# Optimization experiments

Hardware: AMD Instinct MI355X
Metric: run time of the kernel (lower is better)

Reference implementation:

```python
import jax, jax.numpy as jnp
import numpy as np

TEMP = 0.07
BASE_TEMP = 0.07
NUM_HEADS = 8


def setup_inputs() -> dict:
    key = jax.random.key(0)
    k1, k2, k3 = jax.random.split(key, 3)
    B, B2, V, E, C = 1024, 2048, 2, 512, 64
    features = jax.random.normal(k1, (B, V, E), dtype=jnp.float32)
    additional_negatives = jax.random.normal(k2, (B2, V, E), dtype=jnp.float32)
    labels = jax.random.bernoulli(k3, 0.05, (B, C)).astype(jnp.float32)
    return {"features": features, "additional_negatives": additional_negatives, "labels": labels}


def _l2norm(x, eps=1e-12):
    # matches torch.nn.functional.normalize (norm clamped at eps)
    n = jnp.linalg.norm(x, axis=-1, keepdims=True)
    return x / jnp.maximum(n, eps)


def reference(features, additional_negatives, labels):
    B, V, E = features.shape
    H = NUM_HEADS
    F = E // H
    N = B * V

    mask0 = (labels @ labels.T) > 0  # (B, B) label-overlap mask

    # torch.cat(torch.unbind(x, dim=1), dim=0): view-major concat -> (N, E)
    f = jnp.transpose(features, (1, 0, 2)).reshape(N, E).reshape(N, H, F)
    neg = jnp.transpose(additional_negatives, (1, 0, 2))
    M = neg.shape[0] * neg.shape[1]
    neg = neg.reshape(M, E // 1).reshape(M, H, F)

    f = _l2norm(f)
    neg = _l2norm(neg)

    # per-head pairwise similarities (the diagonal(dim1=2,dim2=3) of the full
    # (N,H,N,H) product keeps only matching heads -> einsum over shared h)
    D = jnp.einsum('ihf,jhf->ijh', f, f)      # (N, N, H)
    DN = jnp.einsum('ihf,mhf->imh', f, neg)   # (N, M, H)

    heads = jnp.argmax(D, axis=-1)            # (N, N) per-pair best head

    D = D / TEMP
    DN = DN / TEMP

    # The original builds L[i,k,j] = D[i,j,heads[i,k]]; its max over j and the
    # masked exp-sums depend only on (i, heads[i,k]), so compute per (i, h).
    m1 = jax.lax.stop_gradient(jnp.max(D, axis=1))   # (N, H) = max_j D[i,j,h]
    m2 = jax.lax.stop_gradient(jnp.max(DN, axis=1))  # (N, H) = max_m DN[i,m,h]

    not_self = 1.0 - jnp.eye(N, dtype=D.dtype)       # exclude j == i
    S1 = jnp.sum(jnp.exp(D - m1[:, None, :]) * not_self[:, :, None], axis=1)  # (N, H)
    S2 = jnp.sum(jnp.exp(DN - m2[:, None, :]), axis=1)                         # (N, H)

    # note: original sums exp terms referenced to DIFFERENT maxes (m1 vs m2);
    # reproduce that exactly.
    denom = m1 + jnp.log(S1 + S2)                    # (N, H)

    # diagonal term: D[i,k,heads[i,k]] == max_h D[i,k,h]
    Dmax = jnp.max(D, axis=-1)                       # (N, N)
    denom_ik = jnp.take_along_axis(denom, heads, axis=1)  # (N, N)
    log_prob = Dmax - denom_ik                       # (N, N)

    mask = jnp.tile(mask0, (V, V)).astype(D.dtype) * not_self  # (N, N)
    mean_log_prob_pos = jnp.sum(mask * log_prob, axis=1) / jnp.sum(mask, axis=1)
    loss_vec = -(TEMP / BASE_TEMP) * mean_log_prob_pos          # (N,)

    finite = jnp.isfinite(loss_vec)
    cnt = jnp.sum(finite.astype(loss_vec.dtype))
    loss = jnp.sum(jnp.where(finite, loss_vec, 0.0)) / cnt
    loss = jnp.where(jnp.isnan(loss), jnp.zeros((), loss.dtype), loss)
    return loss
```

## Files before the change

kernel.cpp:

```cpp
#include <hip/hip_runtime.h>

typedef unsigned long long u64;
typedef unsigned short ushort_t;
typedef __bf16 bf16x8 __attribute__((ext_vector_type(8)));
typedef float f32x4 __attribute__((ext_vector_type(4)));

#define NROWS 2048
#define MROWS 4096
#define BLAB  1024
#define INVT  (1.0f / 0.07f)
#define K2    (INVT * 1.4426950408889634f)

__device__ __forceinline__ bf16x8 ldb(const ushort_t* p) {
  return __builtin_bit_cast(bf16x8, *(const uint4*)p);
}

__device__ __forceinline__ ushort_t f2bf(float f) {
  unsigned u = __float_as_uint(f);
  u += 0x7fff + ((u >> 16) & 1);
  return (ushort_t)(u >> 16);
}

__global__ void k_prep(const float* __restrict__ feat, const float* __restrict__ negs,
                       const float* __restrict__ labels,
                       ushort_t* __restrict__ fnb, ushort_t* __restrict__ nnb,
                       u64* __restrict__ lbits, float* __restrict__ zbuf) {
  if (blockIdx.x >= 3072) {
    const int gtid = (blockIdx.x - 3072) * 256 + threadIdx.x;
    if (gtid < 4096) zbuf[gtid] = 0.0f;
    const int wid  = gtid >> 6;
    const int lane = threadIdx.x & 63;
    if (wid < BLAB) {
      float v = labels[wid * 64 + lane];
      u64 msk = __ballot(v != 0.0f);
      if (lane == 0) lbits[wid] = msk;
    }
    return;
  }
  const int wid  = blockIdx.x * 4 + ((threadIdx.x >> 6));
  const int lane = threadIdx.x & 63;
  const int g = lane >> 4, ln = lane & 15;
  const int p = wid * 4 + g;
  const float* src;
  ushort_t* dst;
  if (p < NROWS * 8) {
    const int i = p >> 3, h = p & 7;
    const int b = i & (BLAB - 1), v = i >> 10;
    src = feat + (b * 2 + v) * 512 + h * 64;
    dst = fnb + (h * NROWS + i) * 64;
  } else {
    const int q = p - NROWS * 8;
    const int m = q >> 3, h = q & 7;
    const int b2 = m & 2047, v = m >> 11;
    src = negs + (b2 * 2 + v) * 512 + h * 64;
    dst = nnb + (h * MROWS + m) * 64;
  }
  const float4 x = *(const float4*)(src + 4 * ln);
  float ss = x.x * x.x + x.y * x.y + x.z * x.z + x.w * x.w;
#pragma unroll
  for (int d = 1; d < 16; d <<= 1) ss += __shfl_xor(ss, d, 64);
  const float inv = 1.0f / fmaxf(sqrtf(ss), 1e-12f);
  ushort4 o;
  o.x = f2bf(x.x * inv); o.y = f2bf(x.y * inv);
  o.z = f2bf(x.z * inv); o.w = f2bf(x.w * inv);
  *(ushort4*)(dst + 4 * ln) = o;
}

__device__ __forceinline__ void store_ms4(float mc[4][4], float sa[4][4],
                                          float* __restrict__ gm, float* __restrict__ gs,
                                          int base, int off, int lg, int ln) {
#pragma unroll
  for (int rs = 0; rs < 4; ++rs) {
#pragma unroll
    for (int q = 0; q < 4; ++q) {
      float m = mc[rs][q], s = sa[rs][q];
#pragma unroll
      for (int d = 1; d < 16; d <<= 1) {
        m = fmaxf(m, __shfl_xor(m, d, 64));
        s += __shfl_xor(s, d, 64);
      }
      if (ln == 0) {
        const int row = base + rs * 16 + lg * 4 + q;
        gm[row * 128 + off] = m * INVT;
        gs[row * 128 + off] = s * exp2f((1.0f - m) * K2);
      }
      mc[rs][q] = -3.0e38f; sa[rs][q] = 0.0f;
    }
  }
}

__global__ __launch_bounds__(256, 2) void k_passA(const ushort_t* __restrict__ fnb,
                                                  const ushort_t* __restrict__ nnb,
                                                  float* __restrict__ m1p, float* __restrict__ S1p,
                                                  float* __restrict__ m2p, float* __restrict__ S2p) {
  const int tid  = threadIdx.x;
  const int head = blockIdx.x & 7;
  const int rbk  = (blockIdx.x >> 3) & 7;
  const int js   = blockIdx.x >> 6;
  const int w = tid >> 6, lane = tid & 63, lg = lane >> 4, ln = lane & 15;
  const ushort_t* fh = fnb + head * (NROWS * 64);
  const ushort_t* nh = nnb + head * (MROWS * 64);
  const int base = rbk * 256 + w * 64;
  const int off  = head * 16 + js;
  const int j0 = js * 128;
  const int t0 = js * 256;

  bf16x8 a0[4], a1[4];
#pragma unroll
  for (int rs = 0; rs < 4; ++rs) {
    const ushort_t* ap = fh + (base + rs * 16 + ln) * 64 + lg * 8;
    a0[rs] = ldb(ap); a1[rs] = ldb(ap + 32);
  }
  float mc[4][4], sa[4][4];
#pragma unroll
  for (int rs = 0; rs < 4; ++rs)
#pragma unroll
    for (int q = 0; q < 4; ++q) { mc[rs][q] = -3.0e38f; sa[rs][q] = 0.0f; }

#define TPTR(tt) ((tt) < 8 ? fh + (j0 + (tt) * 16 + ln) * 64 : nh + (t0 + ((tt) - 8) * 16 + ln) * 64)
#define NPTR(tt) (nh + (t0 + ((tt) - 8) * 16 + ln) * 64)
#define LOADT(PA, PB, tt) { const ushort_t* np_ = TPTR(tt); PA = *(const uint4*)(np_ + lg * 8); PB = *(const uint4*)(np_ + 32 + lg * 8); }
#define LOADN(PA, PB, tt) { const ushort_t* np_ = NPTR(tt); PA = *(const uint4*)(np_ + lg * 8); PB = *(const uint4*)(np_ + 32 + lg * 8); }

#define STEP(Pa, Pb, gjb, SELF)                                                              \
  {                                                                                          \
    _Pragma("unroll") for (int rs = 0; rs < 4; ++rs) {                                       \
      f32x4 c = {0.0f, 0.0f, 0.0f, 0.0f};                                                    \
      c = __builtin_amdgcn_mfma_f32_16x16x32_bf16(a0[rs], __builtin_bit_cast(bf16x8, Pa), c, 0, 0, 0); \
      c = __builtin_amdgcn_mfma_f32_16x16x32_bf16(a1[rs], __builtin_bit_cast(bf16x8, Pb), c, 0, 0, 0); \
      _Pragma("unroll") for (int q = 0; q < 4; ++q) {                                        \
        const float cv = c[q];                                                               \
        mc[rs][q] = fmaxf(mc[rs][q], cv);                                                    \
        float e = exp2f(fmaf(cv, K2, -K2));                                                  \
        if (SELF && (base + rs * 16 + lg * 4 + q == (gjb) + ln)) e = 0.0f;                   \
        sa[rs][q] += e;                                                                      \
      }                                                                                      \
    }                                                                                        \
  }

  uint4 P0a, P0b, P1a, P1b, P2a, P2b, P3a, P3b;
  LOADT(P0a, P0b, 0); LOADT(P1a, P1b, 1); LOADT(P2a, P2b, 2); LOADT(P3a, P3b, 3);

#pragma unroll 1
  for (int jj = 0; jj < 8; jj += 4) {
    STEP(P0a, P0b, j0 + jj * 16, 1);        LOADT(P0a, P0b, jj + 4);
    STEP(P1a, P1b, j0 + (jj + 1) * 16, 1);  LOADT(P1a, P1b, jj + 5);
    STEP(P2a, P2b, j0 + (jj + 2) * 16, 1);  LOADT(P2a, P2b, jj + 6);
    STEP(P3a, P3b, j0 + (jj + 3) * 16, 1);  LOADT(P3a, P3b, jj + 7);
  }
  store_ms4(mc, sa, m1p, S1p, base, off, lg, ln);

#pragma unroll 1
  for (int kk = 8; kk < 20; kk += 4) {
    STEP(P0a, P0b, 0, 0);  LOADN(P0a, P0b, kk + 4);
    STEP(P1a, P1b, 0, 0);  LOADN(P1a, P1b, kk + 5);
    STEP(P2a, P2b, 0, 0);  LOADN(P2a, P2b, kk + 6);
    STEP(P3a, P3b, 0, 0);  LOADN(P3a, P3b, kk + 7);
  }
  STEP(P0a, P0b, 0, 0);
  STEP(P1a, P1b, 0, 0);
  STEP(P2a, P2b, 0, 0);
  STEP(P3a, P3b, 0, 0);
  store_ms4(mc, sa, m2p, S2p, base, off, lg, ln);
#undef STEP
#undef LOADT
#undef LOADN
#undef TPTR
#undef NPTR
}

__global__ void k_denom(const float* __restrict__ m1p, const float* __restrict__ S1p,
                        const float* __restrict__ m2p, const float* __restrict__ S2p,
                        float* __restrict__ dnm) {
  const int e = blockIdx.x * 256 + threadIdx.x;
  const int row = e >> 3, h = e & 7;
  const int bidx = row * 128 + h * 16;
  float4 mq[4], sq[4], m2q[4], s2q[4];
#pragma unroll
  for (int k = 0; k < 4; ++k) {
    mq[k]  = *(const float4*)(m1p + bidx + 4 * k);
    sq[k]  = *(const float4*)(S1p + bidx + 4 * k);
    m2q[k] = *(const float4*)(m2p + bidx + 4 * k);
    s2q[k] = *(const float4*)(S2p + bidx + 4 * k);
  }
  float m = -3.0e38f, m2 = -3.0e38f;
#pragma unroll
  for (int k = 0; k < 4; ++k) {
    m  = fmaxf(m,  fmaxf(fmaxf(mq[k].x,  mq[k].y),  fmaxf(mq[k].z,  mq[k].w)));
    m2 = fmaxf(m2, fmaxf(fmaxf(m2q[k].x, m2q[k].y), fmaxf(m2q[k].z, m2q[k].w)));
  }
  float s = 0.0f, s2 = 0.0f;
#pragma unroll
  for (int k = 0; k < 4; ++k) {
    s  += sq[k].x  * __expf(mq[k].x  - m)  + sq[k].y  * __expf(mq[k].y  - m)
        + sq[k].z  * __expf(mq[k].z  - m)  + sq[k].w  * __expf(mq[k].w  - m);
    s2 += s2q[k].x * __expf(m2q[k].x - m2) + s2q[k].y * __expf(m2q[k].y - m2)
        + s2q[k].z * __expf(m2q[k].z - m2) + s2q[k].w * __expf(m2q[k].w - m2);
  }
  dnm[row * 8 + h] = m + __logf(s + s2);
}

__global__ __launch_bounds__(256, 2) void k_passB(const ushort_t* __restrict__ fnb,
                                                  const float* __restrict__ dnm,
                                                  const u64* __restrict__ lbits,
                                                  float* __restrict__ rowsum, float* __restrict__ rowcnt) {
  __shared__ float dn[64 * 9];
  const int tid = threadIdx.x;
  const int it = blockIdx.x >> 5, jt = blockIdx.x & 31;
  const int ibase = it * 64, jbase = jt * 64;
  const int w = tid >> 6, lane = tid & 63, lg = lane >> 4, ln = lane & 15;

  for (int e = tid; e < 512; e += 256) {
    const int il = e >> 3, h = e & 7;
    dn[il * 9 + h] = dnm[(ibase + il) * 8 + h];
  }
  __syncthreads();

  float dnr[4][8];
#pragma unroll
  for (int q = 0; q < 4; ++q) {
    const int il = w * 16 + lg * 4 + q;
#pragma unroll
    for (int h = 0; h < 8; ++h) dnr[q][h] = dn[il * 9 + h];
  }

  const int irow = ibase + w * 16 + ln;
  float maxd[4][4], bestdn[4][4];
#pragma unroll
  for (int sj = 0; sj < 4; ++sj)
#pragma unroll
    for (int q = 0; q < 4; ++q) { maxd[sj][q] = -3.0e38f; bestdn[sj][q] = 0.0f; }

#pragma unroll
  for (int h = 0; h < 8; ++h) {
    const ushort_t* fh = fnb + h * (NROWS * 64);
    const bf16x8 a0 = ldb(fh + irow * 64 + lg * 8);
    const bf16x8 a1 = ldb(fh + irow * 64 + 32 + lg * 8);
#pragma unroll
    for (int sj = 0; sj < 4; ++sj) {
      const int jrow = jbase + sj * 16 + ln;
      const bf16x8 b0 = ldb(fh + jrow * 64 + lg * 8);
      const bf16x8 b1 = ldb(fh + jrow * 64 + 32 + lg * 8);
      f32x4 c = {0.0f, 0.0f, 0.0f, 0.0f};
      c = __builtin_amdgcn_mfma_f32_16x16x32_bf16(a0, b0, c, 0, 0, 0);
      c = __builtin_amdgcn_mfma_f32_16x16x32_bf16(a1, b1, c, 0, 0, 0);
#pragma unroll
      for (int q = 0; q < 4; ++q)
        if (c[q] > maxd[sj][q]) { maxd[sj][q] = c[q]; bestdn[sj][q] = dnr[q][h]; }
    }
  }

  u64 lbi[4];
#pragma unroll
  for (int q = 0; q < 4; ++q) lbi[q] = lbits[(ibase + w * 16 + lg * 4 + q) & (BLAB - 1)];
  float rs[4] = {0, 0, 0, 0}, rc[4] = {0, 0, 0, 0};
#pragma unroll
  for (int sj = 0; sj < 4; ++sj) {
    const int gj = jbase + sj * 16 + ln;
    const u64 lbj = lbits[gj & (BLAB - 1)];
#pragma unroll
    for (int q = 0; q < 4; ++q) {
      const int gi = ibase + w * 16 + lg * 4 + q;
      if (gi != gj && (lbi[q] & lbj)) {
        rs[q] += maxd[sj][q] * INVT - bestdn[sj][q];
        rc[q] += 1.0f;
      }
    }
  }
#pragma unroll
  for (int q = 0; q < 4; ++q) {
#pragma unroll
    for (int d = 1; d < 16; d <<= 1) {
      rs[q] += __shfl_xor(rs[q], d, 64);
      rc[q] += __shfl_xor(rc[q], d, 64);
    }
  }
  if (ln == 0) {
#pragma unroll
    for (int q = 0; q < 4; ++q) {
      const int row = ibase + w * 16 + lg * 4 + q;
      atomicAdd(&rowsum[row], rs[q]);
      atomicAdd(&rowcnt[row], rc[q]);
    }
  }
}

__global__ void k_final(const float* __restrict__ rowsum, const float* __restrict__ rowcnt,
                        float* __restrict__ out) {
  __shared__ float sdata[4][2];
  const int tid = threadIdx.x;
  float s = 0.0f, c = 0.0f;
  for (int i = tid; i < NROWS; i += 256) {
    const float cnt = rowcnt[i];
    if (cnt > 0.0f) { s -= rowsum[i] / cnt; c += 1.0f; }
  }
#pragma unroll
  for (int d = 32; d; d >>= 1) { s += __shfl_xor(s, d, 64); c += __shfl_xor(c, d, 64); }
  const int w = tid >> 6;
  if ((tid & 63) == 0) { sdata[w][0] = s; sdata[w][1] = c; }
  __syncthreads();
  if (tid == 0) {
    s = 0.0f; c = 0.0f;
#pragma unroll
    for (int w2 = 0; w2 < 4; ++w2) { s += sdata[w2][0]; c += sdata[w2][1]; }
    out[0] = (c > 0.0f) ? s / c : 0.0f;
  }
}

extern "C" void kernel_launch(void* const* d_in, const int* in_sizes, int n_in,
                              void* d_out, int out_size, void* d_ws, size_t ws_size,
                              hipStream_t stream) {
  const float* feat   = (const float*)d_in[0];
  const float* negs   = (const float*)d_in[1];
  const float* labels = (const float*)d_in[2];
  float* out = (float*)d_out;

  ushort_t* fnb = (ushort_t*)d_ws;
  ushort_t* nnb = fnb + 8 * NROWS * 64;
  float* m1p = (float*)(nnb + 8 * MROWS * 64);
  float* S1p = m1p + NROWS * 128;
  float* m2p = S1p + NROWS * 128;
  float* S2p = m2p + NROWS * 128;
  float* rowsum = S2p + NROWS * 128;
  float* rowcnt = rowsum + 2048;
  u64*   lbits  = (u64*)(rowcnt + 2048);
  float* dnm    = (float*)(lbits + 1024);

  k_prep<<<3328, 256, 0, stream>>>(feat, negs, labels, fnb, nnb, lbits, rowsum);
  k_passA<<<1024, 256, 0, stream>>>(fnb, nnb, m1p, S1p, m2p, S2p);
  k_denom<<<64, 256, 0, stream>>>(m1p, S1p, m2p, S2p, dnm);
  k_passB<<<1024, 256, 0, stream>>>(fnb, dnm, lbits, rowsum, rowcnt);
  k_final<<<1, 256, 0, stream>>>(rowsum, rowcnt, out);
}
```

Measured before the change: 162.2 us.

## Stage passA B-tiles in swizzled LDS via direct global-to-LDS loads

Instead of each wave streaming the 24 key/negative tiles from global memory into registers with a 4-deep software prefetch, the block now loads all 24 tiles (48 KB) once into shared memory with global_load_lds and an XOR swizzle, then reads them from LDS inside the MFMA loop. This removes redundant per-wave global loads, since all 4 waves share the same B tiles, and avoids bank conflicts through the swizzle. In exchange it uses 48 KB of LDS per block, which may limit occupancy under the 2-blocks-per-SM launch bound. It also serializes all loads before compute with a full wait and barrier, so load latency is no longer overlapped with math.

```diff
diff --git a/kernel.cpp b/kernel.cpp
--- a/kernel.cpp
+++ b/kernel.cpp
@@ -93,6 +93,7 @@
                                                   const ushort_t* __restrict__ nnb,
                                                   float* __restrict__ m1p, float* __restrict__ S1p,
                                                   float* __restrict__ m2p, float* __restrict__ S2p) {
+  __shared__ ushort_t Bs[24 * 1024];
   const int tid  = threadIdx.x;
   const int head = blockIdx.x & 7;
   const int rbk  = (blockIdx.x >> 3) & 7;
@@ -105,6 +106,20 @@
   const int j0 = js * 128;
   const int t0 = js * 256;
 
+  {
+    const int pos  = tid & 127;
+    const int srow = pos >> 3;
+    const int sk   = pos & 7;
+    const int gsw  = (sk ^ (srow & 7)) * 8;
+    for (int r = 0; r < 12; ++r) {
+      const int tl = r * 2 + (tid >> 7);
+      const ushort_t* gsrc = (tl < 8 ? fh + (j0 + tl * 16 + srow) * 64
+                                     : nh + (t0 + (tl - 8) * 16 + srow) * 64) + gsw;
+      __builtin_amdgcn_global_load_lds((const unsigned int*)gsrc,
+                                       (unsigned int*)(Bs + tl * 1024 + pos * 8), 16, 0, 0);
+    }
+  }
+
   bf16x8 a0[4], a1[4];
 #pragma unroll
   for (int rs = 0; rs < 4; ++rs) {
@@ -117,13 +132,14 @@
 #pragma unroll
     for (int q = 0; q < 4; ++q) { mc[rs][q] = -3.0e38f; sa[rs][q] = 0.0f; }
 
-#define TPTR(tt) ((tt) < 8 ? fh + (j0 + (tt) * 16 + ln) * 64 : nh + (t0 + ((tt) - 8) * 16 + ln) * 64)
-#define NPTR(tt) (nh + (t0 + ((tt) - 8) * 16 + ln) * 64)
-#define LOADT(PA, PB, tt) { const ushort_t* np_ = TPTR(tt); PA = *(const uint4*)(np_ + lg * 8); PB = *(const uint4*)(np_ + 32 + lg * 8); }
-#define LOADN(PA, PB, tt) { const ushort_t* np_ = NPTR(tt); PA = *(const uint4*)(np_ + lg * 8); PB = *(const uint4*)(np_ + 32 + lg * 8); }
-
-#define STEP(Pa, Pb, gjb, SELF)                                                              \
+  asm volatile("s_waitcnt vmcnt(0)" ::: "memory");
+  __syncthreads();
+
+#define TCHUNK(tt, c) (Bs + (tt) * 1024 + (ln * 8 + ((c) ^ (ln & 7))) * 8)
+#define STEP(tt, gjb, SELF)                                                                  \
   {                                                                                          \
+    const uint4 Pa = *(const uint4*)TCHUNK(tt, lg);                                          \
+    const uint4 Pb = *(const uint4*)TCHUNK(tt, lg + 4);                                      \
     _Pragma("unroll") for (int rs = 0; rs < 4; ++rs) {                                       \
       f32x4 c = {0.0f, 0.0f, 0.0f, 0.0f};                                                    \
       c = __builtin_amdgcn_mfma_f32_16x16x32_bf16(a0[rs], __builtin_bit_cast(bf16x8, Pa), c, 0, 0, 0); \
@@ -138,35 +154,15 @@
     }                                                                                        \
   }
 
-  uint4 P0a, P0b, P1a, P1b, P2a, P2b, P3a, P3b;
-  LOADT(P0a, P0b, 0); LOADT(P1a, P1b, 1); LOADT(P2a, P2b, 2); LOADT(P3a, P3b, 3);
-
-#pragma unroll 1
-  for (int jj = 0; jj < 8; jj += 4) {
-    STEP(P0a, P0b, j0 + jj * 16, 1);        LOADT(P0a, P0b, jj + 4);
-    STEP(P1a, P1b, j0 + (jj + 1) * 16, 1);  LOADT(P1a, P1b, jj + 5);
-    STEP(P2a, P2b, j0 + (jj + 2) * 16, 1);  LOADT(P2a, P2b, jj + 6);
-    STEP(P3a, P3b, j0 + (jj + 3) * 16, 1);  LOADT(P3a, P3b, jj + 7);
-  }
+#pragma unroll 2
+  for (int tt = 0; tt < 8; ++tt) STEP(tt, j0 + tt * 16, 1);
   store_ms4(mc, sa, m1p, S1p, base, off, lg, ln);
 
-#pragma unroll 1
-  for (int kk = 8; kk < 20; kk += 4) {
-    STEP(P0a, P0b, 0, 0);  LOADN(P0a, P0b, kk + 4);
-    STEP(P1a, P1b, 0, 0);  LOADN(P1a, P1b, kk + 5);
-    STEP(P2a, P2b, 0, 0);  LOADN(P2a, P2b, kk + 6);
-    STEP(P3a, P3b, 0, 0);  LOADN(P3a, P3b, kk + 7);
-  }
-  STEP(P0a, P0b, 0, 0);
-  STEP(P1a, P1b, 0, 0);
-  STEP(P2a, P2b, 0, 0);
-  STEP(P3a, P3b, 0, 0);
+#pragma unroll 4
+  for (int tt = 8; tt < 24; ++tt) STEP(tt, 0, 0);
   store_ms4(mc, sa, m2p, S2p, base, off, lg, ln);
 #undef STEP
-#undef LOADT
-#undef LOADN
-#undef TPTR
-#undef NPTR
+#undef TCHUNK
 }
 
 __global__ void k_denom(const float* __restrict__ m1p, const float* __restrict__ S1p,
```

Result: no change. 159.9 us (-1.4%).
